# Kernel optimization log

Measured on AMD Instinct MI355X. Metric: run time of the kernel, lower is better.

The kernel has to match this reference:

```python
import jax, jax.numpy as jnp
import numpy as np

N, Z_DIM = 131072, 64
K_CODES = 2048
QUANT_TEMP = 0.0  # default T when 'quant_temp' not passed


def setup_inputs() -> dict:
    key = jax.random.key(0)
    k1, k2 = jax.random.split(key)
    z = jax.random.normal(k1, (N, Z_DIM), dtype=jnp.float32)
    e = jax.random.normal(k2, (K_CODES, Z_DIM), dtype=jnp.float32)
    return {"z": z, "e": e}


def reference(z, e):
    # torch.cdist -> euclidean distance matrix [N, K]; argmin over squared
    # distance gives identical indices (sqrt is monotone), so skip the sqrt.
    # ||z - e||^2 = ||z||^2 - 2 z.e^T + ||e||^2
    z_sq = jnp.sum(z * z, axis=1, keepdims=True)          # [N, 1]
    e_sq = jnp.sum(e * e, axis=1)                          # [K]
    d2 = z_sq - 2.0 * (z @ e.T) + e_sq[None, :]            # [N, K]
    min_indices = jnp.argmin(d2, axis=1)                   # [N] int
    z_q = e[min_indices]                                   # gather [N, Z]
    commit_loss = jnp.mean((z - z_q) ** 2)                 # F.mse_loss
    # straight-through: z + (1 - T) * stop_grad(z_q - z), T = 0
    z_out = z + (1.0 - QUANT_TEMP) * jax.lax.stop_gradient(z_q - z)
    return z_out, min_indices, commit_loss
```

## Files before the change

kernel.cpp:

```cpp
#include <hip/hip_runtime.h>


#define N_ROWS 131072
#define ZD 64
#define KCODES 2048
#define RF 2
#define EPS_S 2e-3f
#define FLAG_CAP 32768

using bf16x8  = __attribute__((ext_vector_type(8))) short;
using floatx4 = __attribute__((ext_vector_type(4))) float;

__device__ inline float bf2f(unsigned short u) {
    union { unsigned int i; float f; } c; c.i = ((unsigned int)u) << 16; return c.f;
}
__device__ inline unsigned short f2bf(float x) {
    union { float f; unsigned int i; } c; c.f = x;
    unsigned int b = c.i + 0x7FFFu + ((c.i >> 16) & 1u);
    return (unsigned short)(b >> 16);
}


__global__ void prep_kernel(const float* __restrict__ e, float* __restrict__ ws) {
    int t = threadIdx.x, lane = t & 63, w = t >> 6;
    if (blockIdx.x == 0 && t == 0) { ws[0] = 0.0f; ((unsigned int*)ws)[1] = 0u; }
    int c = blockIdx.x * 4 + w;
    float* esn = ws + 1024;
    double* esq64 = (double*)((char*)ws + 16384);
    unsigned short* et = (unsigned short*)((char*)ws + 32768);
    float* eT = (float*)((char*)ws + 557056);

    float x = e[(size_t)c * ZD + lane];
    unsigned short h = f2bf(x);
    unsigned short l = f2bf(x - bf2f(h));
    size_t base = ((size_t)(c >> 4) << 11) + ((lane >> 3) << 7) + ((c & 15) << 3) + (lane & 7);
    et[base]        = h;
    et[base + 1024] = l;
    eT[lane * KCODES + c] = x;
    double s = (double)x * (double)x;
    for (int off = 1; off < 64; off <<= 1) s += __shfl_xor(s, off, 64);
    if (lane == 0) { esq64[c] = s; esn[c] = (float)(-0.5 * s); }
}

#define COMPUTE(H0, H1, L0, L1, EN, FCOL) do {                               \
    floatx4 _ai = {EN, EN, EN, EN};                                          \
    floatx4 _zi = {0.0f, 0.0f, 0.0f, 0.0f};                                  \
    _Pragma("unroll")                                                        \
    for (int _rf = 0; _rf < RF; _rf++) {                                     \
        floatx4 acc  = _ai;                                                  \
        floatx4 acc2 = _zi;                                                  \
        acc  = __builtin_amdgcn_mfma_f32_16x16x32_bf16(Ah[_rf][0], H0, acc,  0, 0, 0); \
        acc2 = __builtin_amdgcn_mfma_f32_16x16x32_bf16(Ah[_rf][1], H1, acc2, 0, 0, 0); \
        acc  = __builtin_amdgcn_mfma_f32_16x16x32_bf16(Ah[_rf][0], L0, acc,  0, 0, 0); \
        acc2 = __builtin_amdgcn_mfma_f32_16x16x32_bf16(Ah[_rf][1], L1, acc2, 0, 0, 0); \
        acc  = __builtin_amdgcn_mfma_f32_16x16x32_bf16(Al[_rf][0], H0, acc,  0, 0, 0); \
        acc2 = __builtin_amdgcn_mfma_f32_16x16x32_bf16(Al[_rf][1], H1, acc2, 0, 0, 0); \
        _Pragma("unroll")                                                    \
        for (int _r = 0; _r < 4; _r++) {                                     \
            float _s  = acc[_r] + acc2[_r];                                  \
            bool  _gt = _s > mval[_rf][_r];                                  \
            mv2[_rf][_r]  = __builtin_amdgcn_fmed3f(_s, mval[_rf][_r], mv2[_rf][_r]); \
            midx[_rf][_r] = _gt ? (FCOL) : midx[_rf][_r];                    \
            mval[_rf][_r] = fmaxf(_s, mval[_rf][_r]);                       \
        }                                                                    \
    }                                                                        \
} while (0)

#define STAGE(BUF, TILE) do {                                                \
    const char* _src = etiles + ((size_t)((TILE) & 127) << 12)               \
                       + ((size_t)threadIdx.x << 4);                         \
    __builtin_amdgcn_global_load_lds(                                        \
        (const __attribute__((address_space(1))) unsigned int*)_src,         \
        (__attribute__((address_space(3))) unsigned int*)&tilebuf[BUF][w << 10], \
        16, 0, 0);                                                           \
} while (0)

#define ITER(BUF, CT) do {                                                   \
    STAGE((BUF) ^ 1, (CT) + 1);                                              \
    float _en = esn_sm[(CT) * 16 + lrow];                                    \
    bf16x8 h0 = *(const bf16x8*)(const void*)(tilebuf[BUF] + (lane << 4));   \
    bf16x8 h1 = *(const bf16x8*)(const void*)(tilebuf[BUF] + 1024 + (lane << 4)); \
    bf16x8 l0 = *(const bf16x8*)(const void*)(tilebuf[BUF] + 2048 + (lane << 4)); \
    bf16x8 l1 = *(const bf16x8*)(const void*)(tilebuf[BUF] + 3072 + (lane << 4)); \
    COMPUTE(h0, h1, l0, l1, _en, fcol);                                      \
    fcol += 16.0f;                                                           \
    __syncthreads();                                                         \
} while (0)

__global__ __launch_bounds__(256, 4) void vq_mfma(
        const float* __restrict__ z, const float* __restrict__ e,
        float* __restrict__ ws, float* __restrict__ out) {
    const char* etiles = (const char*)ws + 32768;
    unsigned int* cntp  = (unsigned int*)ws + 1;
    unsigned int* flags = (unsigned int*)((char*)ws + 1081344);

    __shared__ __attribute__((aligned(16))) char tilebuf[2][4096];
    __shared__ __attribute__((aligned(16))) float esn_sm[KCODES];

    int lane = threadIdx.x & 63;
    int w    = threadIdx.x >> 6;
    int wid  = blockIdx.x * 4 + w;
    int row0 = wid * (RF * 16);
    int lrow = lane & 15;
    int lq   = lane >> 4;

    {
        const char* esrc = (const char*)ws + 4096 + ((size_t)threadIdx.x << 4);
        __builtin_amdgcn_global_load_lds(
            (const __attribute__((address_space(1))) unsigned int*)esrc,
            (__attribute__((address_space(3))) unsigned int*)((char*)esn_sm + (w << 10)),
            16, 0, 0);
        __builtin_amdgcn_global_load_lds(
            (const __attribute__((address_space(1))) unsigned int*)(esrc + 4096),
            (__attribute__((address_space(3))) unsigned int*)((char*)esn_sm + 4096 + (w << 10)),
            16, 0, 0);
    }
    STAGE(0, 0);

    bf16x8 Ah[RF][2], Al[RF][2];
#pragma unroll
    for (int rf = 0; rf < RF; rf++)
#pragma unroll
        for (int kc = 0; kc < 2; kc++) {
            const float* zp = z + (size_t)(row0 + rf * 16 + lrow) * ZD + kc * 32 + lq * 8;
            float xv[8];
            *(float4*)(void*)&xv[0] = *(const float4*)(const void*)zp;
            *(float4*)(void*)&xv[4] = *(const float4*)(const void*)(zp + 4);
            bf16x8 h, l;
#pragma unroll
            for (int j = 0; j < 8; j++) {
                unsigned short hb = f2bf(xv[j]);
                h[j] = (short)hb;
                l[j] = (short)f2bf(xv[j] - bf2f(hb));
            }
            Ah[rf][kc] = h; Al[rf][kc] = l;
            asm volatile("" : "+v"(Ah[rf][kc]), "+v"(Al[rf][kc]));
        }

    floatx4 mval[RF], mv2[RF], midx[RF];
#pragma unroll
    for (int rf = 0; rf < RF; rf++)
#pragma unroll
        for (int r = 0; r < 4; r++) {
            mval[rf][r] = -3.0e38f; mv2[rf][r] = -3.0e38f; midx[rf][r] = 0.0f;
        }

    float fcol = (float)lrow;
    __syncthreads();

    for (int ct = 0; ct < 128; ct += 2) {
        ITER(0, ct);
        ITER(1, ct + 1);
    }

    float lacc = 0.0f;
#pragma unroll
    for (int rf = 0; rf < RF; rf++)
#pragma unroll
        for (int r = 0; r < 4; r++) {
            float v = mval[rf][r], v2 = mv2[rf][r], fi = midx[rf][r];
            for (int off = 1; off < 16; off <<= 1) {
                float ov  = __shfl_xor(v,  off, 64);
                float ofi = __shfl_xor(fi, off, 64);
                float ov2 = __shfl_xor(v2, off, 64);
                bool take = (ov > v) || ((ov == v) && (ofi < fi));
                float loser = take ? v : ov;
                v2 = fmaxf(fmaxf(v2, ov2), loser);
                v  = take ? ov  : v;
                fi = take ? ofi : fi;
            }
            int row = row0 + rf * 16 + lq * 4 + r;
            int idx = (int)fi;
            float4 ev = ((const float4*)(const void*)(e + (size_t)idx * ZD))[lrow];
            float4 zv = ((const float4*)(const void*)(z + (size_t)row * ZD))[lrow];
            ((float4*)(void*)(out + (size_t)row * ZD))[lrow] = ev;
            float dx = ev.x - zv.x, dy = ev.y - zv.y;
            float dz = ev.z - zv.z, dw = ev.w - zv.w;
            lacc = fmaf(dx, dx, lacc); lacc = fmaf(dy, dy, lacc);
            lacc = fmaf(dz, dz, lacc); lacc = fmaf(dw, dw, lacc);
            if (lrow == 0) {
                out[(size_t)N_ROWS * ZD + row] = fi;
                if (v - v2 < EPS_S) {
                    unsigned int i = atomicAdd(cntp, 1u);
                    if (i < FLAG_CAP) flags[i] = (unsigned int)row;
                }
            }
        }

    for (int off = 1; off < 64; off <<= 1) lacc += __shfl_xor(lacc, off, 64);
    __shared__ float sm[4];
    if (lane == 0) sm[w] = lacc;
    __syncthreads();
    if (threadIdx.x == 0) atomicAdd(ws, sm[0] + sm[1] + sm[2] + sm[3]);
}

__global__ __launch_bounds__(256) void vq_fixup(
        const float* __restrict__ z, const float* __restrict__ e,
        float* __restrict__ ws, float* __restrict__ out) {
    const double* esq64 = (const double*)((const char*)ws + 16384);
    const float* eT = (const float*)((const char*)ws + 557056);
    const unsigned int* flags = (const unsigned int*)((const char*)ws + 1081344);
    unsigned int cnt = ((const unsigned int*)ws)[1];
    if (cnt > FLAG_CAP) cnt = FLAG_CAP;

    if (blockIdx.x == 0 && threadIdx.x == 0)
        out[(size_t)N_ROWS * ZD + N_ROWS] = ws[0] * (1.0f / 8388608.0f);

    __shared__ float zrow[ZD];
    __shared__ double sd[4]; __shared__ int si[4]; __shared__ int sbest;
    int t = threadIdx.x, lane = t & 63, w = t >> 6;

    for (unsigned int u = blockIdx.x; u < cnt; u += gridDim.x) {
        int row = (int)flags[u];
        __syncthreads();
        if (t < ZD) zrow[t] = z[(size_t)row * ZD + t];
        __syncthreads();

        double dacc[8];
#pragma unroll
        for (int j = 0; j < 8; j++) dacc[j] = 0.0;
        for (int k = 0; k < ZD; k++) {
            double zk = (double)zrow[k];
            const float* ek = eT + k * KCODES + t;
#pragma unroll
            for (int j = 0; j < 8; j++)
                dacc[j] = fma(zk, (double)ek[256 * j], dacc[j]);
        }
        double dmin = 1.0e300; int imin = 0;
#pragma unroll
        for (int j = 0; j < 8; j++) {
            int c = t + 256 * j;
            double d = fma(-2.0, dacc[j], esq64[c]);
            if (d < dmin) { dmin = d; imin = c; }
        }
        for (int off = 1; off < 64; off <<= 1) {
            double od = __shfl_xor(dmin, off, 64);
            int    oi = __shfl_xor(imin, off, 64);
            if (od < dmin || (od == dmin && oi < imin)) { dmin = od; imin = oi; }
        }
        if (lane == 0) { sd[w] = dmin; si[w] = imin; }
        __syncthreads();
        if (t == 0) {
            double bd = sd[0]; int bi = si[0];
            for (int q = 1; q < 4; q++)
                if (sd[q] < bd || (sd[q] == bd && si[q] < bi)) { bd = sd[q]; bi = si[q]; }
            sbest = bi;
        }
        __syncthreads();
        int bi = sbest;
        if (t < 16)
            ((float4*)(void*)(out + (size_t)row * ZD))[t] =
                ((const float4*)(const void*)(e + (size_t)bi * ZD))[t];
        if (t == 0) out[(size_t)N_ROWS * ZD + row] = (float)bi;
    }
}

extern "C" void kernel_launch(void* const* d_in, const int* in_sizes, int n_in,
                              void* d_out, int out_size, void* d_ws, size_t ws_size,
                              hipStream_t stream) {
    const float* z = (const float*)d_in[0];
    const float* e = (const float*)d_in[1];
    float* out = (float*)d_out;
    float* ws  = (float*)d_ws;

    prep_kernel<<<dim3(512), dim3(256), 0, stream>>>(e, ws);
    vq_mfma<<<dim3(1024), dim3(256), 0, stream>>>(z, e, ws, out);
    vq_fixup<<<dim3(256), dim3(256), 0, stream>>>(z, e, ws, out);
}
```

Measured before the change: 210.1 us.

## Double row fragments per wave and software-pipeline MFMA with argmax update

```diff
diff --git a/kernel.cpp b/kernel.cpp
--- a/kernel.cpp
+++ b/kernel.cpp
@@ -4,7 +4,7 @@
 #define N_ROWS 131072
 #define ZD 64
 #define KCODES 2048
-#define RF 2
+#define RF 4
 #define EPS_S 2e-3f
 #define FLAG_CAP 32768
 
@@ -42,26 +42,33 @@
     if (lane == 0) { esq64[c] = s; esn[c] = (float)(-0.5 * s); }
 }
 
-#define COMPUTE(H0, H1, L0, L1, EN, FCOL) do {                               \
+#define MFMA_T(H0, H1, L0, L1, EN, NACC, NACC2) do {                         \
     floatx4 _ai = {EN, EN, EN, EN};                                          \
     floatx4 _zi = {0.0f, 0.0f, 0.0f, 0.0f};                                  \
     _Pragma("unroll")                                                        \
     for (int _rf = 0; _rf < RF; _rf++) {                                     \
-        floatx4 acc  = _ai;                                                  \
-        floatx4 acc2 = _zi;                                                  \
-        acc  = __builtin_amdgcn_mfma_f32_16x16x32_bf16(Ah[_rf][0], H0, acc,  0, 0, 0); \
-        acc2 = __builtin_amdgcn_mfma_f32_16x16x32_bf16(Ah[_rf][1], H1, acc2, 0, 0, 0); \
-        acc  = __builtin_amdgcn_mfma_f32_16x16x32_bf16(Ah[_rf][0], L0, acc,  0, 0, 0); \
-        acc2 = __builtin_amdgcn_mfma_f32_16x16x32_bf16(Ah[_rf][1], L1, acc2, 0, 0, 0); \
-        acc  = __builtin_amdgcn_mfma_f32_16x16x32_bf16(Al[_rf][0], H0, acc,  0, 0, 0); \
-        acc2 = __builtin_amdgcn_mfma_f32_16x16x32_bf16(Al[_rf][1], H1, acc2, 0, 0, 0); \
+        floatx4 a1 = _ai;                                                    \
+        floatx4 a2 = _zi;                                                    \
+        a1 = __builtin_amdgcn_mfma_f32_16x16x32_bf16(Ah[_rf][0], H0, a1, 0, 0, 0); \
+        a2 = __builtin_amdgcn_mfma_f32_16x16x32_bf16(Ah[_rf][1], H1, a2, 0, 0, 0); \
+        a1 = __builtin_amdgcn_mfma_f32_16x16x32_bf16(Ah[_rf][0], L0, a1, 0, 0, 0); \
+        a2 = __builtin_amdgcn_mfma_f32_16x16x32_bf16(Ah[_rf][1], L1, a2, 0, 0, 0); \
+        a1 = __builtin_amdgcn_mfma_f32_16x16x32_bf16(Al[_rf][0], H0, a1, 0, 0, 0); \
+        a2 = __builtin_amdgcn_mfma_f32_16x16x32_bf16(Al[_rf][1], H1, a2, 0, 0, 0); \
+        NACC[_rf] = a1; NACC2[_rf] = a2;                                     \
+    }                                                                        \
+} while (0)
+
+#define ARGMAX_T(PACC, PACC2, FPREV) do {                                    \
+    _Pragma("unroll")                                                        \
+    for (int _rf = 0; _rf < RF; _rf++) {                                     \
         _Pragma("unroll")                                                    \
         for (int _r = 0; _r < 4; _r++) {                                     \
-            float _s  = acc[_r] + acc2[_r];                                  \
+            float _s  = PACC[_rf][_r] + PACC2[_rf][_r];                      \
             bool  _gt = _s > mval[_rf][_r];                                  \
             mv2[_rf][_r]  = __builtin_amdgcn_fmed3f(_s, mval[_rf][_r], mv2[_rf][_r]); \
-            midx[_rf][_r] = _gt ? (FCOL) : midx[_rf][_r];                    \
-            mval[_rf][_r] = fmaxf(_s, mval[_rf][_r]);                       \
+            midx[_rf][_r] = _gt ? (FPREV) : midx[_rf][_r];                   \
+            mval[_rf][_r] = fmaxf(_s, mval[_rf][_r]);                        \
         }                                                                    \
     }                                                                        \
 } while (0)
@@ -75,19 +82,25 @@
         16, 0, 0);                                                           \
 } while (0)
 
-#define ITER(BUF, CT) do {                                                   \
+#define READT(BUF, H0, H1, L0, L1) do {                                      \
+    H0 = *(const bf16x8*)(const void*)(tilebuf[BUF] + (lane << 4));          \
+    H1 = *(const bf16x8*)(const void*)(tilebuf[BUF] + 1024 + (lane << 4));   \
+    L0 = *(const bf16x8*)(const void*)(tilebuf[BUF] + 2048 + (lane << 4));   \
+    L1 = *(const bf16x8*)(const void*)(tilebuf[BUF] + 3072 + (lane << 4));   \
+} while (0)
+
+#define ITER_P(BUF, CT, NACC, NACC2, PACC, PACC2) do {                       \
     STAGE((BUF) ^ 1, (CT) + 1);                                              \
     float _en = esn_sm[(CT) * 16 + lrow];                                    \
-    bf16x8 h0 = *(const bf16x8*)(const void*)(tilebuf[BUF] + (lane << 4));   \
-    bf16x8 h1 = *(const bf16x8*)(const void*)(tilebuf[BUF] + 1024 + (lane << 4)); \
-    bf16x8 l0 = *(const bf16x8*)(const void*)(tilebuf[BUF] + 2048 + (lane << 4)); \
-    bf16x8 l1 = *(const bf16x8*)(const void*)(tilebuf[BUF] + 3072 + (lane << 4)); \
-    COMPUTE(h0, h1, l0, l1, _en, fcol);                                      \
-    fcol += 16.0f;                                                           \
+    bf16x8 h0, h1, l0, l1;                                                   \
+    READT(BUF, h0, h1, l0, l1);                                              \
+    MFMA_T(h0, h1, l0, l1, _en, NACC, NACC2);                                \
+    ARGMAX_T(PACC, PACC2, fprev);                                            \
+    fprev += 16.0f;                                                          \
     __syncthreads();                                                         \
 } while (0)
 
-__global__ __launch_bounds__(256, 4) void vq_mfma(
+__global__ __launch_bounds__(256, 2) void vq_mfma(
         const float* __restrict__ z, const float* __restrict__ e,
         float* __restrict__ ws, float* __restrict__ out) {
     const char* etiles = (const char*)ws + 32768;
@@ -145,13 +158,33 @@
             mval[rf][r] = -3.0e38f; mv2[rf][r] = -3.0e38f; midx[rf][r] = 0.0f;
         }
 
-    float fcol = (float)lrow;
+    floatx4 aA[RF], aA2[RF], aB[RF], aB2[RF];
+    float fprev = (float)lrow;
     __syncthreads();
 
-    for (int ct = 0; ct < 128; ct += 2) {
-        ITER(0, ct);
-        ITER(1, ct + 1);
-    }
+    {
+        STAGE(1, 1);
+        float _en = esn_sm[lrow];
+        bf16x8 h0, h1, l0, l1;
+        READT(0, h0, h1, l0, l1);
+        MFMA_T(h0, h1, l0, l1, _en, aA, aA2);
+        __syncthreads();
+    }
+
+    for (int ct = 1; ct < 127; ct += 2) {
+        ITER_P(1, ct,     aB, aB2, aA, aA2);
+        ITER_P(0, ct + 1, aA, aA2, aB, aB2);
+    }
+
+    {
+        float _en = esn_sm[127 * 16 + lrow];
+        bf16x8 h0, h1, l0, l1;
+        READT(1, h0, h1, l0, l1);
+        MFMA_T(h0, h1, l0, l1, _en, aB, aB2);
+        ARGMAX_T(aA, aA2, fprev);
+        fprev += 16.0f;
+    }
+    ARGMAX_T(aB, aB2, fprev);
 
     float lacc = 0.0f;
 #pragma unroll
@@ -264,6 +297,6 @@
     float* ws  = (float*)d_ws;
 
     prep_kernel<<<dim3(512), dim3(256), 0, stream>>>(e, ws);
-    vq_mfma<<<dim3(1024), dim3(256), 0, stream>>>(z, e, ws, out);
+    vq_mfma<<<dim3(512), dim3(256), 0, stream>>>(z, e, ws, out);
     vq_fixup<<<dim3(256), dim3(256), 0, stream>>>(z, e, ws, out);
 }
```

New measurement: 201.7 us. -4.0%, faster.

## Replace split-bf16 distance MFMAs with single-pass fp16 and widen fixup margin

Applied to the files above, without the earlier changes.

```diff
diff --git a/kernel.cpp b/kernel.cpp
--- a/kernel.cpp
+++ b/kernel.cpp
@@ -4,21 +4,12 @@
 #define N_ROWS 131072
 #define ZD 64
 #define KCODES 2048
-#define RF 2
-#define EPS_S 2e-3f
-#define FLAG_CAP 32768
-
-using bf16x8  = __attribute__((ext_vector_type(8))) short;
+#define RF 4
+#define EPS_S 0.03f
+#define FLAG_CAP 65536
+
+using f16x8   = __attribute__((ext_vector_type(8))) _Float16;
 using floatx4 = __attribute__((ext_vector_type(4))) float;
-
-__device__ inline float bf2f(unsigned short u) {
-    union { unsigned int i; float f; } c; c.i = ((unsigned int)u) << 16; return c.f;
-}
-__device__ inline unsigned short f2bf(float x) {
-    union { float f; unsigned int i; } c; c.f = x;
-    unsigned int b = c.i + 0x7FFFu + ((c.i >> 16) & 1u);
-    return (unsigned short)(b >> 16);
-}
 
 
 __global__ void prep_kernel(const float* __restrict__ e, float* __restrict__ ws) {
@@ -31,43 +22,36 @@
     float* eT = (float*)((char*)ws + 557056);
 
     float x = e[(size_t)c * ZD + lane];
-    unsigned short h = f2bf(x);
-    unsigned short l = f2bf(x - bf2f(h));
-    size_t base = ((size_t)(c >> 4) << 11) + ((lane >> 3) << 7) + ((c & 15) << 3) + (lane & 7);
-    et[base]        = h;
-    et[base + 1024] = l;
+    union { _Float16 h; unsigned short u; } cv;
+    cv.h = (_Float16)x;
+    int base = ((c >> 4) << 10) + ((lane >> 3) << 7) + ((c & 15) << 3) + (lane & 7);
+    et[base] = cv.u;
     eT[lane * KCODES + c] = x;
     double s = (double)x * (double)x;
     for (int off = 1; off < 64; off <<= 1) s += __shfl_xor(s, off, 64);
     if (lane == 0) { esq64[c] = s; esn[c] = (float)(-0.5 * s); }
 }
 
-#define COMPUTE(H0, H1, L0, L1, EN, FCOL) do {                               \
+#define COMPUTE(H0, H1, EN, FCOL) do {                                       \
     floatx4 _ai = {EN, EN, EN, EN};                                          \
-    floatx4 _zi = {0.0f, 0.0f, 0.0f, 0.0f};                                  \
     _Pragma("unroll")                                                        \
     for (int _rf = 0; _rf < RF; _rf++) {                                     \
-        floatx4 acc  = _ai;                                                  \
-        floatx4 acc2 = _zi;                                                  \
-        acc  = __builtin_amdgcn_mfma_f32_16x16x32_bf16(Ah[_rf][0], H0, acc,  0, 0, 0); \
-        acc2 = __builtin_amdgcn_mfma_f32_16x16x32_bf16(Ah[_rf][1], H1, acc2, 0, 0, 0); \
-        acc  = __builtin_amdgcn_mfma_f32_16x16x32_bf16(Ah[_rf][0], L0, acc,  0, 0, 0); \
-        acc2 = __builtin_amdgcn_mfma_f32_16x16x32_bf16(Ah[_rf][1], L1, acc2, 0, 0, 0); \
-        acc  = __builtin_amdgcn_mfma_f32_16x16x32_bf16(Al[_rf][0], H0, acc,  0, 0, 0); \
-        acc2 = __builtin_amdgcn_mfma_f32_16x16x32_bf16(Al[_rf][1], H1, acc2, 0, 0, 0); \
+        floatx4 acc;                                                         \
+        acc = __builtin_amdgcn_mfma_f32_16x16x32_f16(Fh[_rf][0], H0, _ai, 0, 0, 0); \
+        acc = __builtin_amdgcn_mfma_f32_16x16x32_f16(Fh[_rf][1], H1, acc, 0, 0, 0); \
         _Pragma("unroll")                                                    \
         for (int _r = 0; _r < 4; _r++) {                                     \
-            float _s  = acc[_r] + acc2[_r];                                  \
+            float _s  = acc[_r];                                             \
             bool  _gt = _s > mval[_rf][_r];                                  \
             mv2[_rf][_r]  = __builtin_amdgcn_fmed3f(_s, mval[_rf][_r], mv2[_rf][_r]); \
             midx[_rf][_r] = _gt ? (FCOL) : midx[_rf][_r];                    \
-            mval[_rf][_r] = fmaxf(_s, mval[_rf][_r]);                       \
+            mval[_rf][_r] = fmaxf(_s, mval[_rf][_r]);                        \
         }                                                                    \
     }                                                                        \
 } while (0)
 
-#define STAGE(BUF, TILE) do {                                                \
-    const char* _src = etiles + ((size_t)((TILE) & 127) << 12)               \
+#define STAGEP(BUF, P) do {                                                  \
+    const char* _src = etiles + ((size_t)((P) & 63) << 12)                   \
                        + ((size_t)threadIdx.x << 4);                         \
     __builtin_amdgcn_global_load_lds(                                        \
         (const __attribute__((address_space(1))) unsigned int*)_src,         \
@@ -75,24 +59,28 @@
         16, 0, 0);                                                           \
 } while (0)
 
-#define ITER(BUF, CT) do {                                                   \
-    STAGE((BUF) ^ 1, (CT) + 1);                                              \
-    float _en = esn_sm[(CT) * 16 + lrow];                                    \
-    bf16x8 h0 = *(const bf16x8*)(const void*)(tilebuf[BUF] + (lane << 4));   \
-    bf16x8 h1 = *(const bf16x8*)(const void*)(tilebuf[BUF] + 1024 + (lane << 4)); \
-    bf16x8 l0 = *(const bf16x8*)(const void*)(tilebuf[BUF] + 2048 + (lane << 4)); \
-    bf16x8 l1 = *(const bf16x8*)(const void*)(tilebuf[BUF] + 3072 + (lane << 4)); \
-    COMPUTE(h0, h1, l0, l1, _en, fcol);                                      \
+#define ITER2(BUF, P) do {                                                   \
+    STAGEP((BUF) ^ 1, (P) + 1);                                              \
+    float _en0 = esn_sm[(P) * 32 + lrow];                                    \
+    float _en1 = esn_sm[(P) * 32 + 16 + lrow];                               \
+    f16x8 h0, h1;                                                            \
+    h0 = *(const f16x8*)(const void*)(tilebuf[BUF] + (lane << 4));           \
+    h1 = *(const f16x8*)(const void*)(tilebuf[BUF] + 1024 + (lane << 4));    \
+    COMPUTE(h0, h1, _en0, fcol);                                             \
+    fcol += 16.0f;                                                           \
+    h0 = *(const f16x8*)(const void*)(tilebuf[BUF] + 2048 + (lane << 4));    \
+    h1 = *(const f16x8*)(const void*)(tilebuf[BUF] + 3072 + (lane << 4));    \
+    COMPUTE(h0, h1, _en1, fcol);                                             \
     fcol += 16.0f;                                                           \
     __syncthreads();                                                         \
 } while (0)
 
-__global__ __launch_bounds__(256, 4) void vq_mfma(
+__global__ __launch_bounds__(256, 2) void vq_mfma(
         const float* __restrict__ z, const float* __restrict__ e,
         float* __restrict__ ws, float* __restrict__ out) {
     const char* etiles = (const char*)ws + 32768;
     unsigned int* cntp  = (unsigned int*)ws + 1;
-    unsigned int* flags = (unsigned int*)((char*)ws + 1081344);
+    unsigned int* flags = (unsigned int*)((char*)ws + 294912);
 
     __shared__ __attribute__((aligned(16))) char tilebuf[2][4096];
     __shared__ __attribute__((aligned(16))) float esn_sm[KCODES];
@@ -103,6 +91,22 @@
     int row0 = wid * (RF * 16);
     int lrow = lane & 15;
     int lq   = lane >> 4;
+
+    f16x8 Fh[RF][2];
+#pragma unroll
+    for (int rf = 0; rf < RF; rf++)
+#pragma unroll
+        for (int kc = 0; kc < 2; kc++) {
+            const float* zp = z + (size_t)(row0 + rf * 16 + lrow) * ZD + kc * 32 + lq * 8;
+            float xv[8];
+            *(float4*)(void*)&xv[0] = *(const float4*)(const void*)zp;
+            *(float4*)(void*)&xv[4] = *(const float4*)(const void*)(zp + 4);
+            f16x8 h;
+#pragma unroll
+            for (int j = 0; j < 8; j++) h[j] = (_Float16)xv[j];
+            Fh[rf][kc] = h;
+            asm volatile("" : "+v"(Fh[rf][kc]));
+        }
 
     {
         const char* esrc = (const char*)ws + 4096 + ((size_t)threadIdx.x << 4);
@@ -115,27 +119,7 @@
             (__attribute__((address_space(3))) unsigned int*)((char*)esn_sm + 4096 + (w << 10)),
             16, 0, 0);
     }
-    STAGE(0, 0);
-
-    bf16x8 Ah[RF][2], Al[RF][2];
-#pragma unroll
-    for (int rf = 0; rf < RF; rf++)
-#pragma unroll
-        for (int kc = 0; kc < 2; kc++) {
-            const float* zp = z + (size_t)(row0 + rf * 16 + lrow) * ZD + kc * 32 + lq * 8;
-            float xv[8];
-            *(float4*)(void*)&xv[0] = *(const float4*)(const void*)zp;
-            *(float4*)(void*)&xv[4] = *(const float4*)(const void*)(zp + 4);
-            bf16x8 h, l;
-#pragma unroll
-            for (int j = 0; j < 8; j++) {
-                unsigned short hb = f2bf(xv[j]);
-                h[j] = (short)hb;
-                l[j] = (short)f2bf(xv[j] - bf2f(hb));
-            }
-            Ah[rf][kc] = h; Al[rf][kc] = l;
-            asm volatile("" : "+v"(Ah[rf][kc]), "+v"(Al[rf][kc]));
-        }
+    STAGEP(0, 0);
 
     floatx4 mval[RF], mv2[RF], midx[RF];
 #pragma unroll
@@ -148,9 +132,9 @@
     float fcol = (float)lrow;
     __syncthreads();
 
-    for (int ct = 0; ct < 128; ct += 2) {
-        ITER(0, ct);
-        ITER(1, ct + 1);
+    for (int p = 0; p < 64; p += 2) {
+        ITER2(0, p);
+        ITER2(1, p + 1);
     }
 
     float lacc = 0.0f;
@@ -199,9 +183,10 @@
         float* __restrict__ ws, float* __restrict__ out) {
     const double* esq64 = (const double*)((const char*)ws + 16384);
     const float* eT = (const float*)((const char*)ws + 557056);
-    const unsigned int* flags = (const unsigned int*)((const char*)ws + 1081344);
+    const unsigned int* flags = (const unsigned int*)((const char*)ws + 294912);
     unsigned int cnt = ((const unsigned int*)ws)[1];
-    if (cnt > FLAG_CAP) cnt = FLAG_CAP;
+    bool allrows = cnt > FLAG_CAP;
+    unsigned int n = allrows ? N_ROWS : cnt;
 
     if (blockIdx.x == 0 && threadIdx.x == 0)
         out[(size_t)N_ROWS * ZD + N_ROWS] = ws[0] * (1.0f / 8388608.0f);
@@ -210,8 +195,8 @@
     __shared__ double sd[4]; __shared__ int si[4]; __shared__ int sbest;
     int t = threadIdx.x, lane = t & 63, w = t >> 6;
 
-    for (unsigned int u = blockIdx.x; u < cnt; u += gridDim.x) {
-        int row = (int)flags[u];
+    for (unsigned int u = blockIdx.x; u < n; u += gridDim.x) {
+        int row = allrows ? (int)u : (int)flags[u];
         __syncthreads();
         if (t < ZD) zrow[t] = z[(size_t)row * ZD + t];
         __syncthreads();
@@ -264,6 +249,6 @@
     float* ws  = (float*)d_ws;
 
     prep_kernel<<<dim3(512), dim3(256), 0, stream>>>(e, ws);
-    vq_mfma<<<dim3(1024), dim3(256), 0, stream>>>(z, e, ws, out);
-    vq_fixup<<<dim3(256), dim3(256), 0, stream>>>(z, e, ws, out);
-}
+    vq_mfma<<<dim3(512), dim3(256), 0, stream>>>(z, e, ws, out);
+    vq_fixup<<<dim3(1024), dim3(256), 0, stream>>>(z, e, ws, out);
+}
```

Result: faster. 203.3 us (-3.2%).
